# Kernel optimization log

Measured on AMD Instinct MI355X. Metric: run time of the kernel, lower is better.

Reference implementation:

```python
import jax, jax.numpy as jnp
import numpy as np

V, E, ENC, D, A = 10000, 512, 2048, 512, 512  # vocab, embed, encoder_dim, decoder_dim, attention_dim
B, L, T = 64, 49, 20


def setup_inputs() -> dict:
    key = jax.random.key(0)
    ks = jax.random.split(key, 20)
    s = lambda k, shape, fan: jax.random.normal(k, shape, jnp.float32) / np.sqrt(fan)
    return {
        "encoder_out": jax.random.normal(ks[0], (B, L, ENC), jnp.float32),
        "captions": jax.random.randint(ks[1], (B, T), 0, V),
        "emb_table": s(ks[2], (V, E), E),
        "W_enc_att": s(ks[3], (ENC, A), ENC), "b_enc_att": jnp.zeros((A,), jnp.float32),
        "W_dec_att": s(ks[4], (D, A), D), "b_dec_att": jnp.zeros((A,), jnp.float32),
        "w_full": s(ks[5], (A,), A), "b_full": jnp.zeros((), jnp.float32),
        "W_ih": s(ks[6], (4 * D, E + ENC), E + ENC), "b_ih": jnp.zeros((4 * D,), jnp.float32),
        "W_hh": s(ks[7], (4 * D, D), D), "b_hh": jnp.zeros((4 * D,), jnp.float32),
        "W_init_h": s(ks[8], (ENC, D), ENC), "b_init_h": jnp.zeros((D,), jnp.float32),
        "W_init_c": s(ks[9], (ENC, D), ENC), "b_init_c": jnp.zeros((D,), jnp.float32),
        "W_out": s(ks[10], (D, V), D), "b_out": jnp.zeros((V,), jnp.float32),
    }


def _decoder(encoder_out, captions, emb_table, W_enc_att, b_enc_att, W_dec_att,
             b_dec_att, w_full, b_full, W_ih, b_ih, W_hh, b_hh,
             W_init_h, b_init_h, W_init_c, b_init_c, W_out, b_out):
    # init hidden/cell from mean encoder features
    mean_enc = encoder_out.mean(axis=1)                      # (B, ENC)
    h = mean_enc @ W_init_h + b_init_h                        # (B, D)
    c = mean_enc @ W_init_c + b_init_c
    # precompute encoder projection for additive attention (shared across steps)
    enc_proj = jnp.einsum('ble,ea->bla', encoder_out, W_enc_att) + b_enc_att  # (B, L, A)
    embeddings = emb_table[captions]                          # (B, T, E)
    emb_seq = jnp.swapaxes(embeddings, 0, 1)                  # (T, B, E)
    Dh = h.shape[-1]

    def step(carry, emb_t):
        h, c = carry
        # additive attention over L=49 locations
        dec_proj = h @ W_dec_att + b_dec_att                  # (B, A)
        att = jax.nn.relu(enc_proj + dec_proj[:, None, :])    # (B, L, A)
        scores = jnp.einsum('bla,a->bl', att, w_full) + b_full
        alpha = jax.nn.softmax(scores, axis=-1)               # (B, L)
        context = jnp.einsum('bl,ble->be', alpha, encoder_out)  # (B, ENC)
        # LSTMCell (PyTorch gate order: i, f, g, o)
        x = jnp.concatenate([emb_t, context], axis=1)         # (B, E+ENC)
        gates = x @ W_ih.T + b_ih + h @ W_hh.T + b_hh         # (B, 4D)
        i, f, g, o = jnp.split(gates, 4, axis=1)
        i, f, o = jax.nn.sigmoid(i), jax.nn.sigmoid(f), jax.nn.sigmoid(o)
        g = jnp.tanh(g)
        c_new = f * c + i * g
        h_new = o * jnp.tanh(c_new)
        # dropout is identity in eval mode
        logits_t = h_new @ W_out + b_out                      # (B, V)
        return (h_new, c_new), (logits_t, alpha)

    (_, _), (logits, alphas) = jax.lax.scan(step, (h, c), emb_seq)
    logits = jnp.swapaxes(logits, 0, 1)                       # (B, T, V)
    alphas = jnp.swapaxes(alphas, 0, 1)                       # (B, T, L)
    return logits, alphas


def reference(encoder_out, captions, emb_table, W_enc_att, b_enc_att, W_dec_att,
              b_dec_att, w_full, b_full, W_ih, b_ih, W_hh, b_hh,
              W_init_h, b_init_h, W_init_c, b_init_c, W_out, b_out):
    return _decoder(encoder_out, captions, emb_table, W_enc_att, b_enc_att,
                    W_dec_att, b_dec_att, w_full, b_full, W_ih, b_ih, W_hh, b_hh,
                    W_init_h, b_init_h, W_init_c, b_init_c, W_out, b_out)
```

## Files before the change

### kernel.cpp

```cpp
#include <hip/hip_runtime.h>
#include <hip/hip_bf16.h>

constexpr int NV   = 10000;
constexpr int NE   = 512;
constexpr int NENC = 2048;
constexpr int ND   = 512;
constexpr int NA   = 512;
constexpr int NB   = 64;
constexpr int NL   = 49;
constexpr int NT   = 20;
constexpr int KX   = NE + NENC + ND;
constexpr int KIH  = NE + NENC;

typedef short bfrag __attribute__((ext_vector_type(8)));
typedef float f32x4 __attribute__((ext_vector_type(4)));

__device__ __forceinline__ float us2f(unsigned short u) {
    union { unsigned int i; float f; } x; x.i = (unsigned int)u << 16; return x.f;
}
__device__ __forceinline__ unsigned short f2us(float f) {
    union { float f_; unsigned int u; } x; x.f_ = f;
    unsigned int r = (x.u + 0x7fffu + ((x.u >> 16) & 1u)) >> 16;
    return (unsigned short)r;
}

__launch_bounds__(256)
__global__ void k_prep(const float* __restrict__ enc, unsigned short* __restrict__ encb,
                       const float* __restrict__ Wih, unsigned short* __restrict__ Wihb,
                       const float* __restrict__ Whh, unsigned short* __restrict__ Whhb,
                       const float* __restrict__ Wh0, const float* __restrict__ Wc0,
                       const float* __restrict__ Wea, const float* __restrict__ Wda,
                       const float* __restrict__ Wout,
                       unsigned short* __restrict__ WicT, unsigned short* __restrict__ WeaT,
                       unsigned short* __restrict__ WdaT, unsigned short* __restrict__ WoutT,
                       unsigned short* __restrict__ meanbf)
{
    int bid = blockIdx.x;
    if (bid < 12416) {
        const float* src; unsigned short* dst;
        if (bid < 6272)       { src = enc; dst = encb; }
        else if (bid < 11392) { src = Wih; dst = Wihb; bid -= 6272; }
        else                  { src = Whh; dst = Whhb; bid -= 11392; }
        const int i = bid * 1024 + threadIdx.x * 4;
        float4 v = *(const float4*)(src + i);
        dst[i + 0] = f2us(v.x); dst[i + 1] = f2us(v.y);
        dst[i + 2] = f2us(v.z); dst[i + 3] = f2us(v.w);
    } else if (bid < 20752) {
        bid -= 12416;
        __shared__ float t[32][33];
        const float* src; unsigned short* dst; int K, N, nCols;
        if (bid < 1024)      { src = Wh0;  dst = WicT;                     K = NENC; N = ND; nCols = 16; }
        else if (bid < 2048) { src = Wc0;  dst = WicT + (size_t)ND * NENC; K = NENC; N = ND; nCols = 16; bid -= 1024; }
        else if (bid < 3072) { src = Wea;  dst = WeaT;                     K = NENC; N = NA; nCols = 16; bid -= 2048; }
        else if (bid < 3328) { src = Wda;  dst = WdaT;                     K = ND;   N = NA; nCols = 16; bid -= 3072; }
        else                 { src = Wout; dst = WoutT;                    K = ND;   N = NV; nCols = 313; bid -= 3328; }
        const int nb = (bid % nCols) * 32, kb = (bid / nCols) * 32;
        const int tx = threadIdx.x & 31, ty = threadIdx.x >> 5;
        #pragma unroll
        for (int i = ty; i < 32; i += 8) {
            int n = nb + tx;
            t[i][tx] = (n < N) ? src[(size_t)(kb + i) * N + n] : 0.f;
        }
        __syncthreads();
        #pragma unroll
        for (int i = ty; i < 32; i += 8) {
            int n = nb + i;
            if (n < N) dst[(size_t)n * K + kb + tx] = f2us(t[tx][i]);
        }
    } else {
        bid -= 20752;
        const int b = bid >> 3;
        const int e = (bid & 7) * 256 + threadIdx.x;
        const float* p = enc + (size_t)b * NL * NENC + e;
        float s = 0.f;
        #pragma unroll 7
        for (int l = 0; l < NL; ++l) s += p[(size_t)l * NENC];
        meanbf[(size_t)b * NENC + e] = f2us(s * (1.0f / NL));
    }
}

__launch_bounds__(512)
__global__ void k_mfma2(const unsigned short* __restrict__ encb,
                        const unsigned short* __restrict__ WeaT,
                        const float* __restrict__ bea,
                        unsigned short* __restrict__ epb,
                        const unsigned short* __restrict__ meanbf,
                        const unsigned short* __restrict__ WicT,
                        const float* __restrict__ bh, const float* __restrict__ bc,
                        unsigned short* __restrict__ hbf, float* __restrict__ c)
{
    __shared__ float comb[4 * 64 * 16];
    const int tid = threadIdx.x;
    const int wave = tid >> 6, lane = tid & 63;
    const int r = lane & 15, quad = lane >> 4;
    if (blockIdx.x < 392) {
        const int j = ((int)blockIdx.x & 7) * 49 + ((int)blockIdx.x >> 3);
        const int ng = j & 7, mg = j >> 3;
        const int ow = wave & 3, kh = wave >> 2;
        const int wm = ow >> 1, wn = ow & 1;
        const int m0 = mg * 64 + wm * 32;
        const int n0 = ng * 64 + wn * 32;
        const int kb = kh * (NENC / 2);
        const unsigned short* ap0 = encb + (size_t)(m0 + r) * NENC + kb + quad * 8;
        const unsigned short* ap1 = ap0 + (size_t)16 * NENC;
        const unsigned short* bp0 = WeaT + (size_t)(n0 + r) * NENC + kb + quad * 8;
        const unsigned short* bp1 = bp0 + (size_t)16 * NENC;
        f32x4 a00 = {0.f,0.f,0.f,0.f}, a01 = {0.f,0.f,0.f,0.f};
        f32x4 a10 = {0.f,0.f,0.f,0.f}, a11 = {0.f,0.f,0.f,0.f};
        #pragma unroll 4
        for (int k = 0; k < NENC / 2; k += 32) {
            bfrag x0 = *(const bfrag*)(ap0 + k);
            bfrag x1 = *(const bfrag*)(ap1 + k);
            bfrag y0 = *(const bfrag*)(bp0 + k);
            bfrag y1 = *(const bfrag*)(bp1 + k);
            a00 = __builtin_amdgcn_mfma_f32_16x16x32_bf16(x0, y0, a00, 0, 0, 0);
            a01 = __builtin_amdgcn_mfma_f32_16x16x32_bf16(x0, y1, a01, 0, 0, 0);
            a10 = __builtin_amdgcn_mfma_f32_16x16x32_bf16(x1, y0, a10, 0, 0, 0);
            a11 = __builtin_amdgcn_mfma_f32_16x16x32_bf16(x1, y1, a11, 0, 0, 0);
        }
        if (kh == 1) {
            float* d = comb + (ow * 64 + lane) * 16;
            #pragma unroll
            for (int i = 0; i < 4; ++i) {
                d[i]      = a00[i];
                d[4 + i]  = a01[i];
                d[8 + i]  = a10[i];
                d[12 + i] = a11[i];
            }
        }
        __syncthreads();
        if (kh == 0) {
            const float* d = comb + (ow * 64 + lane) * 16;
            const float bv0 = bea[n0 + r], bv1 = bea[n0 + 16 + r];
            #pragma unroll
            for (int i = 0; i < 4; ++i) {
                int ma = m0 + quad * 4 + i, mb = ma + 16;
                epb[(size_t)ma * NA + n0 + r]      = f2us(a00[i] + d[i]      + bv0);
                epb[(size_t)ma * NA + n0 + 16 + r] = f2us(a01[i] + d[4 + i]  + bv1);
                epb[(size_t)mb * NA + n0 + r]      = f2us(a10[i] + d[8 + i]  + bv0);
                epb[(size_t)mb * NA + n0 + 16 + r] = f2us(a11[i] + d[12 + i] + bv1);
            }
        }
    } else {
        const int nt = (int)blockIdx.x - 392;
        const int n0 = nt * 16;
        const int mtile = wave & 3, kh = wave >> 2;
        const int m0 = mtile * 16;
        const int kb = kh * (NENC / 2);
        const unsigned short* ap = meanbf + (size_t)(m0 + r) * NENC + kb + quad * 8;
        const unsigned short* bp = WicT   + (size_t)(n0 + r) * NENC + kb + quad * 8;
        f32x4 acc = {0.f, 0.f, 0.f, 0.f};
        #pragma unroll 4
        for (int k = 0; k < NENC / 2; k += 32) {
            bfrag a = *(const bfrag*)(ap + k);
            bfrag b = *(const bfrag*)(bp + k);
            acc = __builtin_amdgcn_mfma_f32_16x16x32_bf16(a, b, acc, 0, 0, 0);
        }
        if (kh == 1) {
            float* d = comb + (mtile * 64 + lane) * 4;
            #pragma unroll
            for (int i = 0; i < 4; ++i) d[i] = acc[i];
        }
        __syncthreads();
        if (kh == 0) {
            const float* d = comb + (mtile * 64 + lane) * 4;
            const int n = n0 + r;
            const bool isC = n >= ND;
            const float bv = isC ? bc[n - ND] : bh[n];
            #pragma unroll
            for (int i = 0; i < 4; ++i) {
                int m = m0 + quad * 4 + i;
                float v = acc[i] + d[i] + bv;
                if (isC) c[(size_t)m * ND + (n - ND)] = v;
                else     hbf[(size_t)m * ND + n] = f2us(v);
            }
        }
    }
}

__device__ __forceinline__ void logits_tasks(int t, int lo, int hi,
    int worker, int nworkers, int wave, int lane,
    const unsigned short* hbf, const unsigned short* WoutT,
    const float* bout, float* out)
{
    const int slot = wave >> 2, w4 = wave & 3;
    const int r = lane & 15, quad = lane >> 4;
    const int m0 = w4 * 16;
    for (int task = lo + worker * 2 + slot; task < hi; task += nworkers * 2) {
        const int n0 = task * 16;
        const unsigned short* ap = hbf + (size_t)(m0 + r) * ND + quad * 8;
        const unsigned short* bp = WoutT + (size_t)(n0 + r) * ND + quad * 8;
        f32x4 acc = {0.f, 0.f, 0.f, 0.f};
        #pragma unroll
        for (int k = 0; k < ND; k += 32) {
            bfrag a = *(const bfrag*)(ap + k);
            bfrag b = *(const bfrag*)(bp + k);
            acc = __builtin_amdgcn_mfma_f32_16x16x32_bf16(a, b, acc, 0, 0, 0);
        }
        const float bv = bout[n0 + r];
        #pragma unroll
        for (int i = 0; i < 4; ++i) {
            int m = m0 + quad * 4 + i;
            out[((size_t)m * NT + t) * NV + n0 + r] = acc[i] + bv;
        }
    }
}

__device__ __forceinline__ void att_body(int t, int b, int tid,
    const unsigned short* hcur, const float* dpg, const unsigned short* epb,
    const unsigned short* encb, const float* wf, const float* bfs,
    const float* embt, const int* caps, unsigned short* x, float* alpha_out,
    float* dp , float* al )
{
    x[(size_t)b * KX + NE + NENC + tid] = hcur[(size_t)b * ND + tid];
    dp[tid] = dpg[(size_t)b * NA + tid];
    const int tok = caps[b * NT + t];
    x[(size_t)b * KX + tid] = f2us(embt[(size_t)tok * NE + tid]);
    __syncthreads();

    const int wave = tid >> 6, lane = tid & 63;
    const float bfull = bfs[0];
    for (int l = wave; l < NL; l += 8) {
        const unsigned short* ep = epb + ((size_t)b * NL + l) * NA;
        float s = 0.f;
        #pragma unroll
        for (int a = lane; a < NA; a += 64) {
            float v = us2f(ep[a]) + dp[a];
            v = v > 0.f ? v : 0.f;
            s = fmaf(v, wf[a], s);
        }
        #pragma unroll
        for (int off = 32; off > 0; off >>= 1) s += __shfl_down(s, off, 64);
        if (lane == 0) al[l] = s + bfull;
    }
    __syncthreads();

    if (tid < 64) {
        float v = (tid < NL) ? al[tid] : -1e30f;
        float m = v;
        #pragma unroll
        for (int off = 32; off > 0; off >>= 1) m = fmaxf(m, __shfl_xor(m, off, 64));
        float e = (tid < NL) ? expf(v - m) : 0.f;
        float s = e;
        #pragma unroll
        for (int off = 32; off > 0; off >>= 1) s += __shfl_xor(s, off, 64);
        float a = e / s;
        if (tid < NL) {
            al[tid] = a;
            alpha_out[((size_t)b * NT + t) * NL + tid] = a;
        }
    }
    __syncthreads();

    {
        const int e = tid * 4;
        const unsigned short* p = encb + (size_t)b * NL * NENC + e;
        float s0 = 0.f, s1 = 0.f, s2 = 0.f, s3 = 0.f;
        #pragma unroll 7
        for (int l = 0; l < NL; ++l) {
            ushort4 v = *(const ushort4*)(p + (size_t)l * NENC);
            float a = al[l];
            s0 = fmaf(a, us2f(v.x), s0);
            s1 = fmaf(a, us2f(v.y), s1);
            s2 = fmaf(a, us2f(v.z), s2);
            s3 = fmaf(a, us2f(v.w), s3);
        }
        unsigned short* xo = x + (size_t)b * KX + NE + e;
        xo[0] = f2us(s0); xo[1] = f2us(s1); xo[2] = f2us(s2); xo[3] = f2us(s3);
    }
}

__launch_bounds__(512)
__global__ void k_att_logits(int t,
                             const unsigned short* __restrict__ hcur,
                             const float* __restrict__ dpg,
                             const unsigned short* __restrict__ epb,
                             const unsigned short* __restrict__ encb,
                             const float* __restrict__ wf,
                             const float* __restrict__ bfs,
                             const float* __restrict__ embt,
                             const int* __restrict__ captions,
                             unsigned short* __restrict__ x,
                             float* __restrict__ alpha_out,
                             const unsigned short* __restrict__ WoutT,
                             const float* __restrict__ bout,
                             float* __restrict__ out)
{
    __shared__ float smem[576];
    const int bid = blockIdx.x, tid = threadIdx.x;
    if (bid < 64) {
        att_body(t, bid, tid, hcur, dpg, epb, encb, wf, bfs,
                 embt, captions, x, alpha_out, smem, smem + 512);
    } else if (t > 0) {
        logits_tasks(t - 1, 0, 384, bid - 64, 192, tid >> 6, tid & 63,
                     hcur, WoutT, bout, out);
    }
}

__launch_bounds__(512)
__global__ void k_gates_lstm(int t,
                             const unsigned short* __restrict__ x,
                             const unsigned short* __restrict__ Wihb,
                             const unsigned short* __restrict__ Whhb,
                             const float* __restrict__ bih, const float* __restrict__ bhh,
                             unsigned short* __restrict__ hnxt, float* __restrict__ c,
                             const unsigned short* __restrict__ hcur,
                             const unsigned short* __restrict__ WoutT,
                             const float* __restrict__ bout,
                             float* __restrict__ out)
{
    __shared__ float part[8 * 4 * 16 * 16];
    const int bid = blockIdx.x;
    const int wave = threadIdx.x >> 6, lane = threadIdx.x & 63;
    if (bid >= 128) {
        if (t > 0)
            logits_tasks(t - 1, 384, 625, bid - 128, 121, wave, lane,
                         hcur, WoutT, bout, out);
        return;
    }
    const int ng = (bid & 7) * 4 + ((bid >> 3) & 3);
    const int mt = bid >> 5;
    const int m0 = mt * 16, n0 = ng * 16;
    const int r = lane & 15, quad = lane >> 4;
    const int k0 = wave * (KX / 8), k1 = k0 + (KX / 8);

    const unsigned short* ap = x + (size_t)(m0 + r) * KX + quad * 8;
    const unsigned short* bpih[4];
    const unsigned short* bphh[4];
    #pragma unroll
    for (int g = 0; g < 4; ++g) {
        bpih[g] = Wihb + (size_t)(g * ND + n0 + r) * KIH + quad * 8;
        bphh[g] = Whhb + (size_t)(g * ND + n0 + r) * ND + quad * 8;
    }
    f32x4 acc[4] = {{0.f,0.f,0.f,0.f},{0.f,0.f,0.f,0.f},
                    {0.f,0.f,0.f,0.f},{0.f,0.f,0.f,0.f}};

    const int kiA = (k1 < KIH) ? k1 : KIH;
    #pragma unroll 4
    for (int k = k0; k < kiA; k += 32) {
        bfrag a = *(const bfrag*)(ap + k);
        #pragma unroll
        for (int g = 0; g < 4; ++g) {
            bfrag b = *(const bfrag*)(bpih[g] + k);
            acc[g] = __builtin_amdgcn_mfma_f32_16x16x32_bf16(a, b, acc[g], 0, 0, 0);
        }
    }
    const int kiB = (k0 > KIH) ? k0 : KIH;
    #pragma unroll 4
    for (int k = kiB; k < k1; k += 32) {
        bfrag a = *(const bfrag*)(ap + k);
        #pragma unroll
        for (int g = 0; g < 4; ++g) {
            bfrag b = *(const bfrag*)(bphh[g] + (k - KIH));
            acc[g] = __builtin_amdgcn_mfma_f32_16x16x32_bf16(a, b, acc[g], 0, 0, 0);
        }
    }

    #pragma unroll
    for (int g = 0; g < 4; ++g)
        #pragma unroll
        for (int i = 0; i < 4; ++i)
            part[((wave * 4 + g) * 16 + quad * 4 + i) * 16 + r] = acc[g][i];
    __syncthreads();

    if (threadIdx.x < 256) {
        const int row = threadIdx.x >> 4, col = threadIdx.x & 15;
        float gs[4];
        #pragma unroll
        for (int g = 0; g < 4; ++g) {
            float v = 0.f;
            #pragma unroll
            for (int w = 0; w < 8; ++w)
                v += part[((w * 4 + g) * 16 + row) * 16 + col];
            gs[g] = v;
        }
        const int d = n0 + col;
        const int m = m0 + row;
        float gi = gs[0] + bih[d]        + bhh[d];
        float gf = gs[1] + bih[d + 512]  + bhh[d + 512];
        float gg = gs[2] + bih[d + 1024] + bhh[d + 1024];
        float go = gs[3] + bih[d + 1536] + bhh[d + 1536];
        float ig = 1.f / (1.f + expf(-gi));
        float fg = 1.f / (1.f + expf(-gf));
        float g  = tanhf(gg);
        float og = 1.f / (1.f + expf(-go));
        float cn = fg * c[(size_t)m * ND + d] + ig * g;
        float hn = og * tanhf(cn);
        c[(size_t)m * ND + d] = cn;
        hnxt[(size_t)m * ND + d] = f2us(hn);
    }
}

__launch_bounds__(512)
__global__ void k_decproj(const unsigned short* __restrict__ hbf,
                          const unsigned short* __restrict__ WdaT,
                          const float* __restrict__ bda, float* __restrict__ dp)
{
    const int wave = threadIdx.x >> 6, lane = threadIdx.x & 63;
    const int slot = wave >> 2, w4 = wave & 3;
    const int tile = blockIdx.x * 2 + slot;
    const int n0 = tile * 16, m0 = w4 * 16;
    const int r = lane & 15, quad = lane >> 4;
    const unsigned short* ap = hbf + (size_t)(m0 + r) * ND + quad * 8;
    const unsigned short* bp = WdaT + (size_t)(n0 + r) * ND + quad * 8;
    f32x4 acc = {0.f, 0.f, 0.f, 0.f};
    #pragma unroll
    for (int k = 0; k < ND; k += 32) {
        bfrag a = *(const bfrag*)(ap + k);
        bfrag b = *(const bfrag*)(bp + k);
        acc = __builtin_amdgcn_mfma_f32_16x16x32_bf16(a, b, acc, 0, 0, 0);
    }
    const float bv = bda[n0 + r];
    #pragma unroll
    for (int i = 0; i < 4; ++i) {
        int m = m0 + quad * 4 + i;
        dp[(size_t)m * NA + n0 + r] = acc[i] + bv;
    }
}

__launch_bounds__(512)
__global__ void k_logits_fin(int t,
                             const unsigned short* __restrict__ hbf,
                             const unsigned short* __restrict__ WoutT,
                             const float* __restrict__ bout,
                             float* __restrict__ out)
{
    logits_tasks(t, 0, 625, blockIdx.x, 313, threadIdx.x >> 6, threadIdx.x & 63,
                 hbf, WoutT, bout, out);
}

extern "C" void kernel_launch(void* const* d_in, const int* in_sizes, int n_in,
                              void* d_out, int out_size, void* d_ws, size_t ws_size,
                              hipStream_t stream) {
    const float* enc  = (const float*)d_in[0];
    const int*   caps = (const int*)d_in[1];
    const float* embt = (const float*)d_in[2];
    const float* Wea  = (const float*)d_in[3];
    const float* bea  = (const float*)d_in[4];
    const float* Wda  = (const float*)d_in[5];
    const float* bda  = (const float*)d_in[6];
    const float* wf   = (const float*)d_in[7];
    const float* bfs  = (const float*)d_in[8];
    const float* Wih  = (const float*)d_in[9];
    const float* bih  = (const float*)d_in[10];
    const float* Whh  = (const float*)d_in[11];
    const float* bhh  = (const float*)d_in[12];
    const float* Wh0  = (const float*)d_in[13];
    const float* bh0  = (const float*)d_in[14];
    const float* Wc0  = (const float*)d_in[15];
    const float* bc0  = (const float*)d_in[16];
    const float* Wout = (const float*)d_in[17];
    const float* bout = (const float*)d_in[18];

    float* out = (float*)d_out;
    float* alpha_out = out + (size_t)NB * NT * NV;

    char* w = (char*)d_ws;
    float* c     = (float*)w;                 w += (size_t)NB * ND * 4;
    float* dp    = (float*)w;                 w += (size_t)NB * NA * 4;
    unsigned short* meanbf = (unsigned short*)w; w += (size_t)NB * NENC * 2;
    unsigned short* hb    = (unsigned short*)w; w += (size_t)2 * NB * ND * 2;
    unsigned short* x     = (unsigned short*)w; w += (size_t)NB * KX * 2;
    unsigned short* epb   = (unsigned short*)w; w += (size_t)NB * NL * NA * 2;
    unsigned short* encb  = (unsigned short*)w; w += (size_t)NB * NL * NENC * 2;
    unsigned short* Wihb  = (unsigned short*)w; w += (size_t)4 * ND * KIH * 2;
    unsigned short* Whhb  = (unsigned short*)w; w += (size_t)4 * ND * ND * 2;
    unsigned short* WeaT  = (unsigned short*)w; w += (size_t)NA * NENC * 2;
    unsigned short* WdaT  = (unsigned short*)w; w += (size_t)NA * ND * 2;
    unsigned short* WoutT = (unsigned short*)w; w += (size_t)NV * ND * 2;
    unsigned short* WicT  = (unsigned short*)w; w += (size_t)2 * ND * NENC * 2;

    hipLaunchKernelGGL(k_prep, dim3(21264), dim3(256), 0, stream,
                       enc, encb, Wih, Wihb, Whh, Whhb,
                       Wh0, Wc0, Wea, Wda, Wout, WicT, WeaT, WdaT, WoutT, meanbf);
    hipLaunchKernelGGL(k_mfma2, dim3(456), dim3(512), 0, stream,
                       encb, WeaT, bea, epb, meanbf, WicT, bh0, bc0, hb, c);
    hipLaunchKernelGGL(k_decproj, dim3(16), dim3(512), 0, stream, hb, WdaT, bda, dp);

    for (int t = 0; t < NT; ++t) {
        unsigned short* hcur = hb + (size_t)(t & 1) * NB * ND;
        unsigned short* hnxt = hb + (size_t)((t + 1) & 1) * NB * ND;
        hipLaunchKernelGGL(k_att_logits, dim3(256), dim3(512), 0, stream,
                           t, hcur, dp, epb, encb, wf, bfs, embt, caps,
                           x, alpha_out, WoutT, bout, out);
        hipLaunchKernelGGL(k_gates_lstm, dim3(249), dim3(512), 0, stream,
                           t, x, Wihb, Whhb, bih, bhh, hnxt, c,
                           hcur, WoutT, bout, out);
        if (t + 1 < NT)
            hipLaunchKernelGGL(k_decproj, dim3(16), dim3(512), 0, stream,
                               hnxt, WdaT, bda, dp);
    }
    hipLaunchKernelGGL(k_logits_fin, dim3(313), dim3(512), 0, stream,
                       NT - 1, hb + (size_t)(NT & 1) * NB * ND, WoutT, bout, out);
}
```

Before: 963.5 us.

## Fuse decoder attention projection into attention kernel, dropping per-step decproj launch

Removes the separate MFMA k_decproj kernel launched once per timestep and instead computes h@W_dec_att inside each attention block, one batch row per block, using scalar FMAs over a bf16 (non-transposed) copy of W_dec_att staged in prep. This eliminates 20 kernel launches and their serialization gaps on the recurrent critical path. In exchange, each of the 64 attention blocks reads the full 512x512 bf16 weight (L2-resident) and does 512 serial FMAs per thread, which lengthens the attention phase. The prep kernel's block ranges are reshuffled to add the Wda cast and drop its transpose.

```diff
diff --git a/kernel.cpp b/kernel.cpp
--- a/kernel.cpp
+++ b/kernel.cpp
@@ -28,32 +28,32 @@
 __global__ void k_prep(const float* __restrict__ enc, unsigned short* __restrict__ encb,
                        const float* __restrict__ Wih, unsigned short* __restrict__ Wihb,
                        const float* __restrict__ Whh, unsigned short* __restrict__ Whhb,
+                       const float* __restrict__ Wda, unsigned short* __restrict__ Wdab,
                        const float* __restrict__ Wh0, const float* __restrict__ Wc0,
-                       const float* __restrict__ Wea, const float* __restrict__ Wda,
-                       const float* __restrict__ Wout,
+                       const float* __restrict__ Wea, const float* __restrict__ Wout,
                        unsigned short* __restrict__ WicT, unsigned short* __restrict__ WeaT,
-                       unsigned short* __restrict__ WdaT, unsigned short* __restrict__ WoutT,
+                       unsigned short* __restrict__ WoutT,
                        unsigned short* __restrict__ meanbf)
 {
     int bid = blockIdx.x;
-    if (bid < 12416) {
+    if (bid < 12672) {
         const float* src; unsigned short* dst;
         if (bid < 6272)       { src = enc; dst = encb; }
         else if (bid < 11392) { src = Wih; dst = Wihb; bid -= 6272; }
-        else                  { src = Whh; dst = Whhb; bid -= 11392; }
+        else if (bid < 12416) { src = Whh; dst = Whhb; bid -= 11392; }
+        else                  { src = Wda; dst = Wdab; bid -= 12416; }
         const int i = bid * 1024 + threadIdx.x * 4;
         float4 v = *(const float4*)(src + i);
         dst[i + 0] = f2us(v.x); dst[i + 1] = f2us(v.y);
         dst[i + 2] = f2us(v.z); dst[i + 3] = f2us(v.w);
     } else if (bid < 20752) {
-        bid -= 12416;
+        bid -= 12672;
         __shared__ float t[32][33];
         const float* src; unsigned short* dst; int K, N, nCols;
         if (bid < 1024)      { src = Wh0;  dst = WicT;                     K = NENC; N = ND; nCols = 16; }
         else if (bid < 2048) { src = Wc0;  dst = WicT + (size_t)ND * NENC; K = NENC; N = ND; nCols = 16; bid -= 1024; }
         else if (bid < 3072) { src = Wea;  dst = WeaT;                     K = NENC; N = NA; nCols = 16; bid -= 2048; }
-        else if (bid < 3328) { src = Wda;  dst = WdaT;                     K = ND;   N = NA; nCols = 16; bid -= 3072; }
-        else                 { src = Wout; dst = WoutT;                    K = ND;   N = NV; nCols = 313; bid -= 3328; }
+        else                 { src = Wout; dst = WoutT;                    K = ND;   N = NV; nCols = 313; bid -= 3072; }
         const int nb = (bid % nCols) * 32, kb = (bid / nCols) * 32;
         const int tx = threadIdx.x & 31, ty = threadIdx.x >> 5;
         #pragma unroll
@@ -207,15 +207,27 @@
 }
 
 __device__ __forceinline__ void att_body(int t, int b, int tid,
-    const unsigned short* hcur, const float* dpg, const unsigned short* epb,
-    const unsigned short* encb, const float* wf, const float* bfs,
+    const unsigned short* hcur, const unsigned short* epb,
+    const unsigned short* encb, const unsigned short* Wdab,
+    const float* bda, const float* wf, const float* bfs,
     const float* embt, const int* caps, unsigned short* x, float* alpha_out,
-    float* dp , float* al )
-{
-    x[(size_t)b * KX + NE + NENC + tid] = hcur[(size_t)b * ND + tid];
-    dp[tid] = dpg[(size_t)b * NA + tid];
+    float* dp , float* al , float* hs )
+{
+    const unsigned short hv = hcur[(size_t)b * ND + tid];
+    x[(size_t)b * KX + NE + NENC + tid] = hv;
+    hs[tid] = us2f(hv);
     const int tok = caps[b * NT + t];
     x[(size_t)b * KX + tid] = f2us(embt[(size_t)tok * NE + tid]);
+    __syncthreads();
+
+    {
+        float acc = 0.f;
+        const unsigned short* wp = Wdab + tid;
+        #pragma unroll 8
+        for (int k = 0; k < ND; ++k)
+            acc = fmaf(hs[k], us2f(wp[(size_t)k * NA]), acc);
+        dp[tid] = acc + bda[tid];
+    }
     __syncthreads();
 
     const int wave = tid >> 6, lane = tid & 63;
@@ -273,9 +285,10 @@
 __launch_bounds__(512)
 __global__ void k_att_logits(int t,
                              const unsigned short* __restrict__ hcur,
-                             const float* __restrict__ dpg,
                              const unsigned short* __restrict__ epb,
                              const unsigned short* __restrict__ encb,
+                             const unsigned short* __restrict__ Wdab,
+                             const float* __restrict__ bda,
                              const float* __restrict__ wf,
                              const float* __restrict__ bfs,
                              const float* __restrict__ embt,
@@ -286,11 +299,11 @@
                              const float* __restrict__ bout,
                              float* __restrict__ out)
 {
-    __shared__ float smem[576];
+    __shared__ float smem[1088];
     const int bid = blockIdx.x, tid = threadIdx.x;
     if (bid < 64) {
-        att_body(t, bid, tid, hcur, dpg, epb, encb, wf, bfs,
-                 embt, captions, x, alpha_out, smem, smem + 512);
+        att_body(t, bid, tid, hcur, epb, encb, Wdab, bda, wf, bfs,
+                 embt, captions, x, alpha_out, smem, smem + 512, smem + 576);
     } else if (t > 0) {
         logits_tasks(t - 1, 0, 384, bid - 64, 192, tid >> 6, tid & 63,
                      hcur, WoutT, bout, out);
@@ -388,33 +401,6 @@
         float hn = og * tanhf(cn);
         c[(size_t)m * ND + d] = cn;
         hnxt[(size_t)m * ND + d] = f2us(hn);
-    }
-}
-
-__launch_bounds__(512)
-__global__ void k_decproj(const unsigned short* __restrict__ hbf,
-                          const unsigned short* __restrict__ WdaT,
-                          const float* __restrict__ bda, float* __restrict__ dp)
-{
-    const int wave = threadIdx.x >> 6, lane = threadIdx.x & 63;
-    const int slot = wave >> 2, w4 = wave & 3;
-    const int tile = blockIdx.x * 2 + slot;
-    const int n0 = tile * 16, m0 = w4 * 16;
-    const int r = lane & 15, quad = lane >> 4;
-    const unsigned short* ap = hbf + (size_t)(m0 + r) * ND + quad * 8;
-    const unsigned short* bp = WdaT + (size_t)(n0 + r) * ND + quad * 8;
-    f32x4 acc = {0.f, 0.f, 0.f, 0.f};
-    #pragma unroll
-    for (int k = 0; k < ND; k += 32) {
-        bfrag a = *(const bfrag*)(ap + k);
-        bfrag b = *(const bfrag*)(bp + k);
-        acc = __builtin_amdgcn_mfma_f32_16x16x32_bf16(a, b, acc, 0, 0, 0);
-    }
-    const float bv = bda[n0 + r];
-    #pragma unroll
-    for (int i = 0; i < 4; ++i) {
-        int m = m0 + quad * 4 + i;
-        dp[(size_t)m * NA + n0 + r] = acc[i] + bv;
     }
 }
 
@@ -457,7 +443,6 @@
 
     char* w = (char*)d_ws;
     float* c     = (float*)w;                 w += (size_t)NB * ND * 4;
-    float* dp    = (float*)w;                 w += (size_t)NB * NA * 4;
     unsigned short* meanbf = (unsigned short*)w; w += (size_t)NB * NENC * 2;
     unsigned short* hb    = (unsigned short*)w; w += (size_t)2 * NB * ND * 2;
     unsigned short* x     = (unsigned short*)w; w += (size_t)NB * KX * 2;
@@ -466,29 +451,25 @@
     unsigned short* Wihb  = (unsigned short*)w; w += (size_t)4 * ND * KIH * 2;
     unsigned short* Whhb  = (unsigned short*)w; w += (size_t)4 * ND * ND * 2;
     unsigned short* WeaT  = (unsigned short*)w; w += (size_t)NA * NENC * 2;
-    unsigned short* WdaT  = (unsigned short*)w; w += (size_t)NA * ND * 2;
+    unsigned short* Wdab  = (unsigned short*)w; w += (size_t)ND * NA * 2;
     unsigned short* WoutT = (unsigned short*)w; w += (size_t)NV * ND * 2;
     unsigned short* WicT  = (unsigned short*)w; w += (size_t)2 * ND * NENC * 2;
 
     hipLaunchKernelGGL(k_prep, dim3(21264), dim3(256), 0, stream,
-                       enc, encb, Wih, Wihb, Whh, Whhb,
-                       Wh0, Wc0, Wea, Wda, Wout, WicT, WeaT, WdaT, WoutT, meanbf);
+                       enc, encb, Wih, Wihb, Whh, Whhb, Wda, Wdab,
+                       Wh0, Wc0, Wea, Wout, WicT, WeaT, WoutT, meanbf);
     hipLaunchKernelGGL(k_mfma2, dim3(456), dim3(512), 0, stream,
                        encb, WeaT, bea, epb, meanbf, WicT, bh0, bc0, hb, c);
-    hipLaunchKernelGGL(k_decproj, dim3(16), dim3(512), 0, stream, hb, WdaT, bda, dp);
 
     for (int t = 0; t < NT; ++t) {
         unsigned short* hcur = hb + (size_t)(t & 1) * NB * ND;
         unsigned short* hnxt = hb + (size_t)((t + 1) & 1) * NB * ND;
         hipLaunchKernelGGL(k_att_logits, dim3(256), dim3(512), 0, stream,
-                           t, hcur, dp, epb, encb, wf, bfs, embt, caps,
+                           t, hcur, epb, encb, Wdab, bda, wf, bfs, embt, caps,
                            x, alpha_out, WoutT, bout, out);
         hipLaunchKernelGGL(k_gates_lstm, dim3(249), dim3(512), 0, stream,
                            t, x, Wihb, Whhb, bih, bhh, hnxt, c,
                            hcur, WoutT, bout, out);
-        if (t + 1 < NT)
-            hipLaunchKernelGGL(k_decproj, dim3(16), dim3(512), 0, stream,
-                               hnxt, WdaT, bda, dp);
     }
     hipLaunchKernelGGL(k_logits_fin, dim3(313), dim3(512), 0, stream,
                        NT - 1, hb + (size_t)(NT & 1) * NB * ND, WoutT, bout, out);
```

Measured after the change: 1.152 ms. 1.2x slower.

## Fuse decoder-projection kernel into attention kernel with global flag synchronization

Applied to the files above, without the earlier changes.

Removes the separate k_decproj launch per timestep and computes the decoder attention projection in the first 16 blocks of k_att_logits. The attention blocks spin on a per-timestep atomic counter until all 16 projection blocks have published their results, then read dp. This removes 20 kernel launches and their serialization gaps, but it depends on the producer blocks being scheduled alongside the spinning consumers. If they are not co-resident, the spin-wait could deadlock.

```diff
diff --git a/kernel.cpp b/kernel.cpp
--- a/kernel.cpp
+++ b/kernel.cpp
@@ -33,7 +33,7 @@
                        const float* __restrict__ Wout,
                        unsigned short* __restrict__ WicT, unsigned short* __restrict__ WeaT,
                        unsigned short* __restrict__ WdaT, unsigned short* __restrict__ WoutT,
-                       unsigned short* __restrict__ meanbf)
+                       unsigned short* __restrict__ meanbf, int* __restrict__ flags)
 {
     int bid = blockIdx.x;
     if (bid < 12416) {
@@ -67,7 +67,7 @@
             int n = nb + i;
             if (n < N) dst[(size_t)n * K + kb + tx] = f2us(t[tx][i]);
         }
-    } else {
+    } else if (bid < 21264) {
         bid -= 20752;
         const int b = bid >> 3;
         const int e = (bid & 7) * 256 + threadIdx.x;
@@ -76,6 +76,8 @@
         #pragma unroll 7
         for (int l = 0; l < NL; ++l) s += p[(size_t)l * NENC];
         meanbf[(size_t)b * NENC + e] = f2us(s * (1.0f / NL));
+    } else {
+        if (threadIdx.x < NT) flags[threadIdx.x] = 0;
     }
 }
 
@@ -210,12 +212,22 @@
     const unsigned short* hcur, const float* dpg, const unsigned short* epb,
     const unsigned short* encb, const float* wf, const float* bfs,
     const float* embt, const int* caps, unsigned short* x, float* alpha_out,
+    int* flags,
     float* dp , float* al )
 {
     x[(size_t)b * KX + NE + NENC + tid] = hcur[(size_t)b * ND + tid];
-    dp[tid] = dpg[(size_t)b * NA + tid];
     const int tok = caps[b * NT + t];
     x[(size_t)b * KX + tid] = f2us(embt[(size_t)tok * NE + tid]);
+
+    if ((tid & 63) == 0) {
+        while (__hip_atomic_load(&flags[t], __ATOMIC_RELAXED,
+                                 __HIP_MEMORY_SCOPE_AGENT) < 16)
+            __builtin_amdgcn_s_sleep(2);
+    }
+    __syncthreads();
+    (void)__hip_atomic_load(&flags[t], __ATOMIC_ACQUIRE, __HIP_MEMORY_SCOPE_AGENT);
+
+    dp[tid] = dpg[(size_t)b * NA + tid];
     __syncthreads();
 
     const int wave = tid >> 6, lane = tid & 63;
@@ -273,7 +285,9 @@
 __launch_bounds__(512)
 __global__ void k_att_logits(int t,
                              const unsigned short* __restrict__ hcur,
-                             const float* __restrict__ dpg,
+                             float* __restrict__ dp,
+                             const unsigned short* __restrict__ WdaT,
+                             const float* __restrict__ bda,
                              const unsigned short* __restrict__ epb,
                              const unsigned short* __restrict__ encb,
                              const float* __restrict__ wf,
@@ -284,15 +298,42 @@
                              float* __restrict__ alpha_out,
                              const unsigned short* __restrict__ WoutT,
                              const float* __restrict__ bout,
-                             float* __restrict__ out)
+                             float* __restrict__ out,
+                             int* __restrict__ flags)
 {
     __shared__ float smem[576];
     const int bid = blockIdx.x, tid = threadIdx.x;
-    if (bid < 64) {
-        att_body(t, bid, tid, hcur, dpg, epb, encb, wf, bfs,
-                 embt, captions, x, alpha_out, smem, smem + 512);
+    const int wave = tid >> 6, lane = tid & 63;
+    if (bid < 16) {
+        const int slot = wave >> 2, w4 = wave & 3;
+        const int tile = bid * 2 + slot;
+        const int n0 = tile * 16, m0 = w4 * 16;
+        const int r = lane & 15, quad = lane >> 4;
+        const unsigned short* ap = hcur + (size_t)(m0 + r) * ND + quad * 8;
+        const unsigned short* bp = WdaT + (size_t)(n0 + r) * ND + quad * 8;
+        f32x4 acc = {0.f, 0.f, 0.f, 0.f};
+        #pragma unroll
+        for (int k = 0; k < ND; k += 32) {
+            bfrag a = *(const bfrag*)(ap + k);
+            bfrag b = *(const bfrag*)(bp + k);
+            acc = __builtin_amdgcn_mfma_f32_16x16x32_bf16(a, b, acc, 0, 0, 0);
+        }
+        const float bv = bda[n0 + r];
+        #pragma unroll
+        for (int i = 0; i < 4; ++i) {
+            int m = m0 + quad * 4 + i;
+            dp[(size_t)m * NA + n0 + r] = acc[i] + bv;
+        }
+        __threadfence();
+        __syncthreads();
+        if (tid == 0)
+            __hip_atomic_fetch_add(&flags[t], 1, __ATOMIC_RELEASE,
+                                   __HIP_MEMORY_SCOPE_AGENT);
+    } else if (bid < 80) {
+        att_body(t, bid - 16, tid, hcur, dp, epb, encb, wf, bfs,
+                 embt, captions, x, alpha_out, flags, smem, smem + 512);
     } else if (t > 0) {
-        logits_tasks(t - 1, 0, 384, bid - 64, 192, tid >> 6, tid & 63,
+        logits_tasks(t - 1, 0, 384, bid - 80, 192, wave, lane,
                      hcur, WoutT, bout, out);
     }
 }
@@ -388,33 +429,6 @@
         float hn = og * tanhf(cn);
         c[(size_t)m * ND + d] = cn;
         hnxt[(size_t)m * ND + d] = f2us(hn);
-    }
-}
-
-__launch_bounds__(512)
-__global__ void k_decproj(const unsigned short* __restrict__ hbf,
-                          const unsigned short* __restrict__ WdaT,
-                          const float* __restrict__ bda, float* __restrict__ dp)
-{
-    const int wave = threadIdx.x >> 6, lane = threadIdx.x & 63;
-    const int slot = wave >> 2, w4 = wave & 3;
-    const int tile = blockIdx.x * 2 + slot;
-    const int n0 = tile * 16, m0 = w4 * 16;
-    const int r = lane & 15, quad = lane >> 4;
-    const unsigned short* ap = hbf + (size_t)(m0 + r) * ND + quad * 8;
-    const unsigned short* bp = WdaT + (size_t)(n0 + r) * ND + quad * 8;
-    f32x4 acc = {0.f, 0.f, 0.f, 0.f};
-    #pragma unroll
-    for (int k = 0; k < ND; k += 32) {
-        bfrag a = *(const bfrag*)(ap + k);
-        bfrag b = *(const bfrag*)(bp + k);
-        acc = __builtin_amdgcn_mfma_f32_16x16x32_bf16(a, b, acc, 0, 0, 0);
-    }
-    const float bv = bda[n0 + r];
-    #pragma unroll
-    for (int i = 0; i < 4; ++i) {
-        int m = m0 + quad * 4 + i;
-        dp[(size_t)m * NA + n0 + r] = acc[i] + bv;
     }
 }
 
@@ -469,26 +483,24 @@
     unsigned short* WdaT  = (unsigned short*)w; w += (size_t)NA * ND * 2;
     unsigned short* WoutT = (unsigned short*)w; w += (size_t)NV * ND * 2;
     unsigned short* WicT  = (unsigned short*)w; w += (size_t)2 * ND * NENC * 2;
-
-    hipLaunchKernelGGL(k_prep, dim3(21264), dim3(256), 0, stream,
+    int* flags = (int*)w;                     w += 64;
+
+    hipLaunchKernelGGL(k_prep, dim3(21265), dim3(256), 0, stream,
                        enc, encb, Wih, Wihb, Whh, Whhb,
-                       Wh0, Wc0, Wea, Wda, Wout, WicT, WeaT, WdaT, WoutT, meanbf);
+                       Wh0, Wc0, Wea, Wda, Wout, WicT, WeaT, WdaT, WoutT,
+                       meanbf, flags);
     hipLaunchKernelGGL(k_mfma2, dim3(456), dim3(512), 0, stream,
                        encb, WeaT, bea, epb, meanbf, WicT, bh0, bc0, hb, c);
-    hipLaunchKernelGGL(k_decproj, dim3(16), dim3(512), 0, stream, hb, WdaT, bda, dp);
 
     for (int t = 0; t < NT; ++t) {
         unsigned short* hcur = hb + (size_t)(t & 1) * NB * ND;
         unsigned short* hnxt = hb + (size_t)((t + 1) & 1) * NB * ND;
-        hipLaunchKernelGGL(k_att_logits, dim3(256), dim3(512), 0, stream,
-                           t, hcur, dp, epb, encb, wf, bfs, embt, caps,
-                           x, alpha_out, WoutT, bout, out);
+        hipLaunchKernelGGL(k_att_logits, dim3(272), dim3(512), 0, stream,
+                           t, hcur, dp, WdaT, bda, epb, encb, wf, bfs, embt, caps,
+                           x, alpha_out, WoutT, bout, out, flags);
         hipLaunchKernelGGL(k_gates_lstm, dim3(249), dim3(512), 0, stream,
                            t, x, Wihb, Whhb, bih, bhh, hnxt, c,
                            hcur, WoutT, bout, out);
-        if (t + 1 < NT)
-            hipLaunchKernelGGL(k_decproj, dim3(16), dim3(512), 0, stream,
-                               hnxt, WdaT, bda, dp);
     }
     hipLaunchKernelGGL(k_logits_fin, dim3(313), dim3(512), 0, stream,
                        NT - 1, hb + (size_t)(NT & 1) * NB * ND, WoutT, bout, out);
```

Measured after the change: 1.148 ms. 1.19x slower.

## Stage encoder-projection GEMM through double-buffered LDS and pre-gather embeddings

Applied to the files above, without the earlier changes.

The encoder-attention projection GEMM now loads 64x64 A and B tiles cooperatively into double-buffered shared memory with register prefetch, instead of each wave streaming its fragments straight from global memory. Both K-halves read from the same staged tile. Separately, all caption embeddings are gathered and converted to bf16 once in the prep kernel. The per-step concatenated x buffer is dropped, so the LSTM gate kernel reads embedding, context and h from separate buffers. This removes per-step copies, at the cost of a sync per K-slice in the GEMM and a branch in the gate A-load.

```diff
diff --git a/kernel.cpp b/kernel.cpp
--- a/kernel.cpp
+++ b/kernel.cpp
@@ -33,7 +33,9 @@
                        const float* __restrict__ Wout,
                        unsigned short* __restrict__ WicT, unsigned short* __restrict__ WeaT,
                        unsigned short* __restrict__ WdaT, unsigned short* __restrict__ WoutT,
-                       unsigned short* __restrict__ meanbf)
+                       unsigned short* __restrict__ meanbf,
+                       const float* __restrict__ embt, const int* __restrict__ caps,
+                       unsigned short* __restrict__ embs)
 {
     int bid = blockIdx.x;
     if (bid < 12416) {
@@ -67,7 +69,7 @@
             int n = nb + i;
             if (n < N) dst[(size_t)n * K + kb + tx] = f2us(t[tx][i]);
         }
-    } else {
+    } else if (bid < 21264) {
         bid -= 20752;
         const int b = bid >> 3;
         const int e = (bid & 7) * 256 + threadIdx.x;
@@ -76,6 +78,13 @@
         #pragma unroll 7
         for (int l = 0; l < NL; ++l) s += p[(size_t)l * NENC];
         meanbf[(size_t)b * NENC + e] = f2us(s * (1.0f / NL));
+    } else {
+        bid -= 21264;
+        const int t = bid >> 6, b = bid & 63;
+        const int tok = caps[b * NT + t];
+        float2 v = *(const float2*)(embt + (size_t)tok * NE + threadIdx.x * 2);
+        unsigned short* d = embs + ((size_t)t * NB + b) * NE + threadIdx.x * 2;
+        d[0] = f2us(v.x); d[1] = f2us(v.y);
     }
 }
 
@@ -89,35 +98,61 @@
                         const float* __restrict__ bh, const float* __restrict__ bc,
                         unsigned short* __restrict__ hbf, float* __restrict__ c)
 {
-    __shared__ float comb[4 * 64 * 16];
+    __shared__ short lds_s[2][2][64 * 72];
+    float* comb = (float*)lds_s;
     const int tid = threadIdx.x;
     const int wave = tid >> 6, lane = tid & 63;
     const int r = lane & 15, quad = lane >> 4;
+
     if (blockIdx.x < 392) {
         const int j = ((int)blockIdx.x & 7) * 49 + ((int)blockIdx.x >> 3);
         const int ng = j & 7, mg = j >> 3;
+        const int m0 = mg * 64, n0 = ng * 64;
         const int ow = wave & 3, kh = wave >> 2;
         const int wm = ow >> 1, wn = ow & 1;
-        const int m0 = mg * 64 + wm * 32;
-        const int n0 = ng * 64 + wn * 32;
-        const int kb = kh * (NENC / 2);
-        const unsigned short* ap0 = encb + (size_t)(m0 + r) * NENC + kb + quad * 8;
-        const unsigned short* ap1 = ap0 + (size_t)16 * NENC;
-        const unsigned short* bp0 = WeaT + (size_t)(n0 + r) * NENC + kb + quad * 8;
-        const unsigned short* bp1 = bp0 + (size_t)16 * NENC;
+
+        const int grow = tid >> 3, gcb = tid & 7;
+        const unsigned short* gA = encb + (size_t)(m0 + grow) * NENC + gcb * 8;
+        const unsigned short* gB = WeaT + (size_t)(n0 + grow) * NENC + gcb * 8;
+        const int lidx = grow * 72 + gcb * 8;
+
+        bfrag rA = *(const bfrag*)(gA);
+        bfrag rB = *(const bfrag*)(gB);
+        *(bfrag*)&lds_s[0][0][lidx] = rA;
+        *(bfrag*)&lds_s[0][1][lidx] = rB;
+        rA = *(const bfrag*)(gA + 64);
+        rB = *(const bfrag*)(gB + 64);
+        __syncthreads();
+
         f32x4 a00 = {0.f,0.f,0.f,0.f}, a01 = {0.f,0.f,0.f,0.f};
         f32x4 a10 = {0.f,0.f,0.f,0.f}, a11 = {0.f,0.f,0.f,0.f};
-        #pragma unroll 4
-        for (int k = 0; k < NENC / 2; k += 32) {
-            bfrag x0 = *(const bfrag*)(ap0 + k);
-            bfrag x1 = *(const bfrag*)(ap1 + k);
-            bfrag y0 = *(const bfrag*)(bp0 + k);
-            bfrag y1 = *(const bfrag*)(bp1 + k);
+        const int la0 = (wm * 32 + r) * 72 + kh * 32 + quad * 8;
+        const int la1 = la0 + 16 * 72;
+        const int lb0 = (wn * 32 + r) * 72 + kh * 32 + quad * 8;
+        const int lb1 = lb0 + 16 * 72;
+
+        #pragma unroll 2
+        for (int s = 0; s < 32; ++s) {
+            const int buf = s & 1;
+            if (s + 1 < 32) {
+                *(bfrag*)&lds_s[buf ^ 1][0][lidx] = rA;
+                *(bfrag*)&lds_s[buf ^ 1][1][lidx] = rB;
+            }
+            if (s + 2 < 32) {
+                rA = *(const bfrag*)(gA + (s + 2) * 64);
+                rB = *(const bfrag*)(gB + (s + 2) * 64);
+            }
+            bfrag x0 = *(const bfrag*)&lds_s[buf][0][la0];
+            bfrag x1 = *(const bfrag*)&lds_s[buf][0][la1];
+            bfrag y0 = *(const bfrag*)&lds_s[buf][1][lb0];
+            bfrag y1 = *(const bfrag*)&lds_s[buf][1][lb1];
             a00 = __builtin_amdgcn_mfma_f32_16x16x32_bf16(x0, y0, a00, 0, 0, 0);
             a01 = __builtin_amdgcn_mfma_f32_16x16x32_bf16(x0, y1, a01, 0, 0, 0);
             a10 = __builtin_amdgcn_mfma_f32_16x16x32_bf16(x1, y0, a10, 0, 0, 0);
             a11 = __builtin_amdgcn_mfma_f32_16x16x32_bf16(x1, y1, a11, 0, 0, 0);
-        }
+            __syncthreads();
+        }
+
         if (kh == 1) {
             float* d = comb + (ow * 64 + lane) * 16;
             #pragma unroll
@@ -131,14 +166,15 @@
         __syncthreads();
         if (kh == 0) {
             const float* d = comb + (ow * 64 + lane) * 16;
-            const float bv0 = bea[n0 + r], bv1 = bea[n0 + 16 + r];
+            const int nb0 = n0 + wn * 32;
+            const float bv0 = bea[nb0 + r], bv1 = bea[nb0 + 16 + r];
             #pragma unroll
             for (int i = 0; i < 4; ++i) {
-                int ma = m0 + quad * 4 + i, mb = ma + 16;
-                epb[(size_t)ma * NA + n0 + r]      = f2us(a00[i] + d[i]      + bv0);
-                epb[(size_t)ma * NA + n0 + 16 + r] = f2us(a01[i] + d[4 + i]  + bv1);
-                epb[(size_t)mb * NA + n0 + r]      = f2us(a10[i] + d[8 + i]  + bv0);
-                epb[(size_t)mb * NA + n0 + 16 + r] = f2us(a11[i] + d[12 + i] + bv1);
+                int ma = m0 + wm * 32 + quad * 4 + i, mb = ma + 16;
+                epb[(size_t)ma * NA + nb0 + r]      = f2us(a00[i] + d[i]      + bv0);
+                epb[(size_t)ma * NA + nb0 + 16 + r] = f2us(a01[i] + d[4 + i]  + bv1);
+                epb[(size_t)mb * NA + nb0 + r]      = f2us(a10[i] + d[8 + i]  + bv0);
+                epb[(size_t)mb * NA + nb0 + 16 + r] = f2us(a11[i] + d[12 + i] + bv1);
             }
         }
     } else {
@@ -207,15 +243,11 @@
 }
 
 __device__ __forceinline__ void att_body(int t, int b, int tid,
-    const unsigned short* hcur, const float* dpg, const unsigned short* epb,
-    const unsigned short* encb, const float* wf, const float* bfs,
-    const float* embt, const int* caps, unsigned short* x, float* alpha_out,
+    const float* dpg, const unsigned short* epb, const unsigned short* encb,
+    const float* wf, const float* bfs, unsigned short* ctx, float* alpha_out,
     float* dp , float* al )
 {
-    x[(size_t)b * KX + NE + NENC + tid] = hcur[(size_t)b * ND + tid];
     dp[tid] = dpg[(size_t)b * NA + tid];
-    const int tok = caps[b * NT + t];
-    x[(size_t)b * KX + tid] = f2us(embt[(size_t)tok * NE + tid]);
     __syncthreads();
 
     const int wave = tid >> 6, lane = tid & 63;
@@ -265,7 +297,7 @@
             s2 = fmaf(a, us2f(v.z), s2);
             s3 = fmaf(a, us2f(v.w), s3);
         }
-        unsigned short* xo = x + (size_t)b * KX + NE + e;
+        unsigned short* xo = ctx + (size_t)b * NENC + e;
         xo[0] = f2us(s0); xo[1] = f2us(s1); xo[2] = f2us(s2); xo[3] = f2us(s3);
     }
 }
@@ -278,9 +310,7 @@
                              const unsigned short* __restrict__ encb,
                              const float* __restrict__ wf,
                              const float* __restrict__ bfs,
-                             const float* __restrict__ embt,
-                             const int* __restrict__ captions,
-                             unsigned short* __restrict__ x,
+                             unsigned short* __restrict__ ctx,
                              float* __restrict__ alpha_out,
                              const unsigned short* __restrict__ WoutT,
                              const float* __restrict__ bout,
@@ -289,8 +319,8 @@
     __shared__ float smem[576];
     const int bid = blockIdx.x, tid = threadIdx.x;
     if (bid < 64) {
-        att_body(t, bid, tid, hcur, dpg, epb, encb, wf, bfs,
-                 embt, captions, x, alpha_out, smem, smem + 512);
+        att_body(t, bid, tid, dpg, epb, encb, wf, bfs, ctx, alpha_out,
+                 smem, smem + 512);
     } else if (t > 0) {
         logits_tasks(t - 1, 0, 384, bid - 64, 192, tid >> 6, tid & 63,
                      hcur, WoutT, bout, out);
@@ -299,7 +329,8 @@
 
 __launch_bounds__(512)
 __global__ void k_gates_lstm(int t,
-                             const unsigned short* __restrict__ x,
+                             const unsigned short* __restrict__ embs,
+                             const unsigned short* __restrict__ ctx,
                              const unsigned short* __restrict__ Wihb,
                              const unsigned short* __restrict__ Whhb,
                              const float* __restrict__ bih, const float* __restrict__ bhh,
@@ -324,7 +355,10 @@
     const int r = lane & 15, quad = lane >> 4;
     const int k0 = wave * (KX / 8), k1 = k0 + (KX / 8);
 
-    const unsigned short* ap = x + (size_t)(m0 + r) * KX + quad * 8;
+    const int arow = m0 + r;
+    const unsigned short* aE = embs + ((size_t)t * NB + arow) * NE + quad * 8;
+    const unsigned short* aC = ctx + (size_t)arow * NENC + quad * 8;
+    const unsigned short* aH = hcur + (size_t)arow * ND + quad * 8;
     const unsigned short* bpih[4];
     const unsigned short* bphh[4];
     #pragma unroll
@@ -338,7 +372,8 @@
     const int kiA = (k1 < KIH) ? k1 : KIH;
     #pragma unroll 4
     for (int k = k0; k < kiA; k += 32) {
-        bfrag a = *(const bfrag*)(ap + k);
+        bfrag a = (k < NE) ? *(const bfrag*)(aE + k)
+                           : *(const bfrag*)(aC + (k - NE));
         #pragma unroll
         for (int g = 0; g < 4; ++g) {
             bfrag b = *(const bfrag*)(bpih[g] + k);
@@ -348,7 +383,7 @@
     const int kiB = (k0 > KIH) ? k0 : KIH;
     #pragma unroll 4
     for (int k = kiB; k < k1; k += 32) {
-        bfrag a = *(const bfrag*)(ap + k);
+        bfrag a = *(const bfrag*)(aH + (k - KIH));
         #pragma unroll
         for (int g = 0; g < 4; ++g) {
             bfrag b = *(const bfrag*)(bphh[g] + (k - KIH));
@@ -460,7 +495,8 @@
     float* dp    = (float*)w;                 w += (size_t)NB * NA * 4;
     unsigned short* meanbf = (unsigned short*)w; w += (size_t)NB * NENC * 2;
     unsigned short* hb    = (unsigned short*)w; w += (size_t)2 * NB * ND * 2;
-    unsigned short* x     = (unsigned short*)w; w += (size_t)NB * KX * 2;
+    unsigned short* ctx   = (unsigned short*)w; w += (size_t)NB * NENC * 2;
+    unsigned short* embs  = (unsigned short*)w; w += (size_t)NT * NB * NE * 2;
     unsigned short* epb   = (unsigned short*)w; w += (size_t)NB * NL * NA * 2;
     unsigned short* encb  = (unsigned short*)w; w += (size_t)NB * NL * NENC * 2;
     unsigned short* Wihb  = (unsigned short*)w; w += (size_t)4 * ND * KIH * 2;
@@ -470,9 +506,10 @@
     unsigned short* WoutT = (unsigned short*)w; w += (size_t)NV * ND * 2;
     unsigned short* WicT  = (unsigned short*)w; w += (size_t)2 * ND * NENC * 2;
 
-    hipLaunchKernelGGL(k_prep, dim3(21264), dim3(256), 0, stream,
+    hipLaunchKernelGGL(k_prep, dim3(22544), dim3(256), 0, stream,
                        enc, encb, Wih, Wihb, Whh, Whhb,
-                       Wh0, Wc0, Wea, Wda, Wout, WicT, WeaT, WdaT, WoutT, meanbf);
+                       Wh0, Wc0, Wea, Wda, Wout, WicT, WeaT, WdaT, WoutT,
+                       meanbf, embt, caps, embs);
     hipLaunchKernelGGL(k_mfma2, dim3(456), dim3(512), 0, stream,
                        encb, WeaT, bea, epb, meanbf, WicT, bh0, bc0, hb, c);
     hipLaunchKernelGGL(k_decproj, dim3(16), dim3(512), 0, stream, hb, WdaT, bda, dp);
@@ -481,10 +518,10 @@
         unsigned short* hcur = hb + (size_t)(t & 1) * NB * ND;
         unsigned short* hnxt = hb + (size_t)((t + 1) & 1) * NB * ND;
         hipLaunchKernelGGL(k_att_logits, dim3(256), dim3(512), 0, stream,
-                           t, hcur, dp, epb, encb, wf, bfs, embt, caps,
-                           x, alpha_out, WoutT, bout, out);
+                           t, hcur, dp, epb, encb, wf, bfs, ctx, alpha_out,
+                           WoutT, bout, out);
         hipLaunchKernelGGL(k_gates_lstm, dim3(249), dim3(512), 0, stream,
-                           t, x, Wihb, Whhb, bih, bhh, hnxt, c,
+                           t, embs, ctx, Wihb, Whhb, bih, bhh, hnxt, c,
                            hcur, WoutT, bout, out);
         if (t + 1 < NT)
             hipLaunchKernelGGL(k_decproj, dim3(16), dim3(512), 0, stream,
```

Result: faster. 933.0 us (-3.2%).
